# Performance work log

Measured on AMD Instinct MI355X. Metric: run time of the kernel, lower is better.

## Reference

```python
import jax, jax.numpy as jnp
import numpy as np

H = 1024
NH = 16
HD = H // NH

def setup_inputs() -> dict:
    key = jax.random.key(0)
    ks = jax.random.split(key, 8)
    s = 1.0 / np.sqrt(H)
    hidden_states = jax.random.normal(ks[0], (2, 2048, H), dtype=jnp.float32)
    attention_mask = jnp.zeros((2, 1, 1, 2048), dtype=jnp.float32)
    Wq = jax.random.uniform(ks[1], (H, H), jnp.float32, -s, s)
    bq = jax.random.uniform(ks[2], (H,), jnp.float32, -s, s)
    Wk = jax.random.uniform(ks[3], (H, H), jnp.float32, -s, s)
    bk = jax.random.uniform(ks[4], (H,), jnp.float32, -s, s)
    Wv = jax.random.uniform(ks[5], (H, H), jnp.float32, -s, s)
    bv = jax.random.uniform(ks[6], (H,), jnp.float32, -s, s)
    return {"hidden_states": hidden_states, "attention_mask": attention_mask,
            "Wq": Wq, "bq": bq, "Wk": Wk, "bk": bk, "Wv": Wv, "bv": bv}

def _split_heads(x):
    B, L, _ = x.shape
    return x.reshape(B, L, NH, HD).transpose(0, 2, 1, 3)  # [B, nh, L, hd]

def reference(hidden_states, attention_mask, Wq, bq, Wk, bk, Wv, bv):
    # QKV projections (nn.Linear: x @ W.T + b)
    Q = _split_heads(hidden_states @ Wq.T + bq)
    K = _split_heads(hidden_states @ Wk.T + bk)
    V = _split_heads(hidden_states @ Wv.T + bv)
    scale = 1.0 / np.sqrt(HD)
    scores = jnp.einsum('bhqd,bhkd->bhqk', Q, K) * scale  # [B, nh, L, L]
    scores = scores + attention_mask
    probs = jax.nn.softmax(scores, axis=-1)  # dropout in eval mode = identity
    context = jnp.einsum('bhqk,bhkd->bhqd', probs, V)
    B, _, L, _ = context.shape
    return context.transpose(0, 2, 1, 3).reshape(B, L, H)
```

## Files before the change

kernel.cpp:

```cpp
#include <hip/hip_runtime.h>
#include <math.h>
#include <stdint.h>

#define H_DIM 1024
#define NH 16
#define HD 64
#define B_DIM 2
#define L_DIM 2048
#define M_TOT (B_DIM * L_DIM)

typedef __bf16 bf16_t;
typedef __bf16 bf16x8 __attribute__((ext_vector_type(8)));
typedef __bf16 bf16x4 __attribute__((ext_vector_type(4)));
typedef float  f32x4  __attribute__((ext_vector_type(4)));

#define AS1 const __attribute__((address_space(1))) void*
#define AS3 __attribute__((address_space(3))) void*

__global__ __launch_bounds__(256)
void cast_all(const float* __restrict__ x,
              const float* __restrict__ Wq, const float* __restrict__ Wk,
              const float* __restrict__ Wv, bf16_t* __restrict__ dst)
{
    const size_t idx = ((size_t)blockIdx.x * 256 + threadIdx.x) * 4;
    const float* src;
    size_t off;
    if (idx < (size_t)M_TOT * H_DIM) { src = x; off = idx; }
    else {
        size_t j = idx - (size_t)M_TOT * H_DIM;
        int z = (int)(j >> 20);
        off = j & ((1u << 20) - 1);
        src = (z == 0) ? Wq : (z == 1) ? Wk : Wv;
    }
    const float4 v = *(const float4*)(src + off);
    bf16x4 o;
    o[0] = (bf16_t)v.x; o[1] = (bf16_t)v.y;
    o[2] = (bf16_t)v.z; o[3] = (bf16_t)v.w;
    *(bf16x4*)(dst + idx) = o;
}

__global__ __launch_bounds__(256, 1)
void qkv_mfma(const bf16_t* __restrict__ xb, const bf16_t* __restrict__ wb,
              const float* __restrict__ bq, const float* __restrict__ bk,
              const float* __restrict__ bv,
              bf16_t* __restrict__ qb, bf16_t* __restrict__ kb,
              bf16_t* __restrict__ vt)
{
    __shared__ bf16_t As0[128 * 32];
    __shared__ bf16_t As1[128 * 32];
    __shared__ bf16_t As2[128 * 32];
    __shared__ bf16_t Bs0[3][128 * 32];
    __shared__ bf16_t Bs1[3][128 * 32];
    __shared__ bf16_t Bs2[3][128 * 32];

    const int tid = threadIdx.x;
    const int n   = blockIdx.x;
    const int bn  = (n & 7) * 128;
    const int bm  = (n >> 3) * 128;

    const int wave = tid >> 6;
    const int lane = tid & 63;
    const int lc   = lane & 15;
    const int quad = lane >> 4;
    const int wm   = wave >> 1;
    const int wn   = wave & 1;

    f32x4 acc[3][4][4];
    #pragma unroll
    for (int z = 0; z < 3; ++z)
        #pragma unroll
        for (int i = 0; i < 4; ++i)
            #pragma unroll
            for (int j = 0; j < 4; ++j)
                acc[z][i][j] = (f32x4){0.f, 0.f, 0.f, 0.f};

    const int srow = tid >> 2;
    const int sseg = tid & 3;
    const bf16_t* gA = xb + (size_t)(bm + srow) * H_DIM + (sseg ^ (srow & 3)) * 8;
    const bf16_t* gB = wb + (size_t)(bn + srow) * H_DIM + (sseg ^ (srow & 3)) * 8;
    const int woff = wave * 1024;

    auto stage = [&](int k0, bf16_t* A_, bf16_t (*B_)[128 * 32]) {
        __builtin_amdgcn_global_load_lds((AS1)(gA + k0),
            (AS3)((char*)A_ + woff), 16, 0, 0);
        __builtin_amdgcn_global_load_lds((AS1)(gA + k0 + (size_t)64 * H_DIM),
            (AS3)((char*)A_ + woff + 4096), 16, 0, 0);
        #pragma unroll
        for (int z = 0; z < 3; ++z) {
            const bf16_t* g = gB + (size_t)z * H_DIM * H_DIM + k0;
            __builtin_amdgcn_global_load_lds((AS1)(g),
                (AS3)((char*)B_[z] + woff), 16, 0, 0);
            __builtin_amdgcn_global_load_lds((AS1)(g + (size_t)64 * H_DIM),
                (AS3)((char*)B_[z] + woff + 4096), 16, 0, 0);
        }
    };

    const int slot = (quad ^ (lc & 3)) * 8;
    auto compute = [&](const bf16_t* A_, const bf16_t (*B_)[128 * 32]) {
        bf16x8 a[4];
        #pragma unroll
        for (int mi = 0; mi < 4; ++mi)
            a[mi] = *(const bf16x8*)(A_ + (wm * 64 + mi * 16 + lc) * 32 + slot);
        #pragma unroll
        for (int z = 0; z < 3; ++z) {
            bf16x8 b[4];
            #pragma unroll
            for (int ni = 0; ni < 4; ++ni)
                b[ni] = *(const bf16x8*)(B_[z] + (wn * 64 + ni * 16 + lc) * 32 + slot);
            #pragma unroll
            for (int mi = 0; mi < 4; ++mi)
                #pragma unroll
                for (int ni = 0; ni < 4; ++ni)
                    acc[z][mi][ni] = __builtin_amdgcn_mfma_f32_16x16x32_bf16(
                        a[mi], b[ni], acc[z][mi][ni], 0, 0, 0);
        }
    };

    auto step = [&](int kk, bf16_t* cA, bf16_t (*cB)[128 * 32],
                    bf16_t* nA, bf16_t (*nB)[128 * 32], bool doStage) {
        __builtin_amdgcn_s_waitcnt(0x0F78);
        __builtin_amdgcn_s_barrier();
        if (doStage) stage((kk + 2) * 32, nA, nB);
        compute(cA, cB);
    };

    stage(0,  As0, Bs0);
    stage(32, As1, Bs1);
    #pragma unroll 1
    for (int t = 0; t < 10; ++t) {
        const int kk = t * 3;
        step(kk,     As0, Bs0, As2, Bs2, true);
        step(kk + 1, As1, Bs1, As0, Bs0, true);
        step(kk + 2, As2, Bs2, As1, Bs1, true);
    }
    step(30, As0, Bs0, As2, Bs2, false);
    __builtin_amdgcn_s_waitcnt(0x0F70);
    __builtin_amdgcn_s_barrier();
    compute(As1, Bs1);

    const int nb = bn + wn * 64;
    #pragma unroll
    for (int z = 0; z < 3; ++z) {
        const float* bias = (z == 0) ? bq : (z == 1) ? bk : bv;
        float biasv[4];
        #pragma unroll
        for (int ni = 0; ni < 4; ++ni) biasv[ni] = bias[nb + ni * 16 + lc];

        #pragma unroll
        for (int mi = 0; mi < 4; ++mi) {
            const int m0 = bm + wm * 64 + mi * 16 + quad * 4;
            if (z == 2) {
                const int b_ = m0 >> 11;
                const int l0 = m0 & 2047;
                #pragma unroll
                for (int ni = 0; ni < 4; ++ni) {
                    const int nn = nb + ni * 16 + lc;
                    const int h = nn >> 6, d = nn & 63;
                    bf16x4 pk;
                    #pragma unroll
                    for (int r = 0; r < 4; ++r)
                        pk[r] = (bf16_t)(acc[z][mi][ni][r] + biasv[ni]);
                    *(bf16x4*)(vt + (((size_t)(b_ * NH + h)) * HD + d) * L_DIM + l0) = pk;
                }
            } else {
                bf16_t* dst = (z == 0) ? qb : kb;
                #pragma unroll
                for (int r = 0; r < 4; ++r) {
                    const int m  = m0 + r;
                    const int b_ = m >> 11;
                    const int l  = m & 2047;
                    #pragma unroll
                    for (int ni = 0; ni < 4; ++ni) {
                        const int nn = nb + ni * 16 + lc;
                        const int h = nn >> 6, d = nn & 63;
                        dst[(((size_t)(b_ * NH + h)) * L_DIM + l) * HD + d] =
                            (bf16_t)(acc[z][mi][ni][r] + biasv[ni]);
                    }
                }
            }
        }
    }
}

#define EXP_C   0.180336879f
#define LOG2E   1.442695041f
#define EXP_SH  11.541560327f

__device__ __forceinline__ void attn_tile32(
    int kbase, bool pre,
    const bf16_t* curK, const bf16_t* curV,
    bf16_t* nxtK, bf16_t* nxtV,
    const bf16_t* gK, const bf16_t* gV,
    bf16_t* Ps, const float* mrow, int lc, int quad,
    const bf16x8 (&bQ)[2][2], f32x4 (&o)[2][4], float (&rs)[2])
{
    __builtin_amdgcn_s_waitcnt(0x0F70);

    const int e = lc & 7;

    bf16x8 kf[2][2];
    #pragma unroll
    for (int ni = 0; ni < 2; ++ni) {
        const bf16_t* p = curK + (ni * 16 + lc) * 64;
        kf[ni][0] = *(const bf16x8*)(p + ((quad ^ e) << 3));
        kf[ni][1] = *(const bf16x8*)(p + (((quad ^ e) ^ 4) << 3));
    }

    if (pre) {
        const int nk = kbase + 32;
        #pragma unroll
        for (int i = 0; i < 4; ++i) {
            __builtin_amdgcn_global_load_lds(
                (AS1)(gK + (size_t)nk * 64 + i * 512),
                (AS3)(nxtK + i * 512), 16, 0, 0);
            __builtin_amdgcn_global_load_lds(
                (AS1)(gV + nk + i * 32768),
                (AS3)(nxtV + i * 512), 16, 0, 0);
        }
    }

    float mvs[2][4];
    #pragma unroll
    for (int ni = 0; ni < 2; ++ni) {
        const float4 mv = *(const float4*)(mrow + kbase + ni * 16 + quad * 4);
        mvs[ni][0] = mv.x * LOG2E - EXP_SH;
        mvs[ni][1] = mv.y * LOG2E - EXP_SH;
        mvs[ni][2] = mv.z * LOG2E - EXP_SH;
        mvs[ni][3] = mv.w * LOG2E - EXP_SH;
    }

    #pragma unroll
    for (int f = 0; f < 2; ++f) {
        f32x4 s[2];
        #pragma unroll
        for (int ni = 0; ni < 2; ++ni) {
            f32x4 t = (f32x4){0.f, 0.f, 0.f, 0.f};
            t = __builtin_amdgcn_mfma_f32_16x16x32_bf16(kf[ni][0], bQ[f][0], t, 0, 0, 0);
            t = __builtin_amdgcn_mfma_f32_16x16x32_bf16(kf[ni][1], bQ[f][1], t, 0, 0, 0);
            s[ni] = t;
        }
        float acc = 0.f;
        #pragma unroll
        for (int ni = 0; ni < 2; ++ni) {
            bf16x4 pk;
            #pragma unroll
            for (int r = 0; r < 4; ++r) {
                const float p = __builtin_amdgcn_exp2f(s[ni][r] * EXP_C + mvs[ni][r]);
                acc += p;
                pk[r] = (bf16_t)p;
            }
            const int c = f * 4 + ni * 2 + (quad >> 1);
            *(bf16x4*)(Ps + lc * 64 + ((c ^ e) << 3) + ((quad & 1) << 2)) = pk;
        }
        rs[f] += acc;
    }

    bf16x8 vf[4];
    const int e2 = lc >> 1;
    #pragma unroll
    for (int dg = 0; dg < 4; ++dg) {
        const int p  = dg * 8 + (lc >> 1);
        const int ch = (((lc & 1) << 2) + quad) ^ e2;
        vf[dg] = *(const bf16x8*)(curV + p * 64 + (ch << 3));
    }

    #pragma unroll
    for (int f = 0; f < 2; ++f) {
        const int c = f * 4 + quad;
        const bf16x8 bP = *(const bf16x8*)(Ps + lc * 64 + ((c ^ e) << 3));
        #pragma unroll
        for (int dg = 0; dg < 4; ++dg)
            o[f][dg] = __builtin_amdgcn_mfma_f32_16x16x32_bf16(vf[dg], bP, o[f][dg], 0, 0, 0);
    }
}

__global__ __launch_bounds__(64, 2)
void attn_mfma(const bf16_t* __restrict__ qb, const bf16_t* __restrict__ kb,
               const bf16_t* __restrict__ vt, const float* __restrict__ mask,
               float* __restrict__ out)
{
    __shared__ bf16_t Ks0[32 * 64];
    __shared__ bf16_t Ks1[32 * 64];
    __shared__ bf16_t Vs0[32 * 64];
    __shared__ bf16_t Vs1[32 * 64];
    __shared__ bf16_t Ps[16 * 64];

    const int lane = threadIdx.x & 63;
    const int lc   = lane & 15;
    const int quad = lane >> 4;
    const int rl   = lane >> 3;
    const int sg   = lane & 7;

    const int n    = blockIdx.x;
    const int bh   = (n & 7) * 4 + ((n >> 3) & 3);
    const int q0   = (n >> 5) * 32;
    const int b_   = bh >> 4;
    const int h    = bh & 15;

    bf16x8 bQ[2][2];
    #pragma unroll
    for (int f = 0; f < 2; ++f) {
        const bf16_t* Qp = qb + ((size_t)bh * L_DIM + q0 + f * 16 + lc) * HD + quad * 8;
        bQ[f][0] = *(const bf16x8*)(Qp);
        bQ[f][1] = *(const bf16x8*)(Qp + 32);
    }

    const bf16_t* Kbase = kb + (size_t)bh * L_DIM * HD;
    const bf16_t* Vbase = vt + (size_t)bh * HD * L_DIM;
    const float*  mrow  = mask + (size_t)b_ * L_DIM;

    const bf16_t* gK = Kbase + rl * 64 + (sg ^ rl) * 8;
    const int cV = sg ^ rl;
    const bf16_t* gV = Vbase + (size_t)(rl * 2 + (cV >> 2)) * L_DIM + (cV & 3) * 8;

    f32x4 o[2][4];
    #pragma unroll
    for (int f = 0; f < 2; ++f)
        #pragma unroll
        for (int dg = 0; dg < 4; ++dg) o[f][dg] = (f32x4){0.f, 0.f, 0.f, 0.f};
    float rs[2] = {0.f, 0.f};

    #pragma unroll
    for (int i = 0; i < 4; ++i) {
        __builtin_amdgcn_global_load_lds(
            (AS1)(gK + i * 512),
            (AS3)(Ks0 + i * 512), 16, 0, 0);
        __builtin_amdgcn_global_load_lds(
            (AS1)(gV + i * 32768),
            (AS3)(Vs0 + i * 512), 16, 0, 0);
    }

    #pragma unroll 1
    for (int t2 = 0; t2 < 32; ++t2) {
        const int kb0 = t2 * 64;
        attn_tile32(kb0,      true,     Ks0, Vs0, Ks1, Vs1, gK, gV, Ps,
                    mrow, lc, quad, bQ, o, rs);
        attn_tile32(kb0 + 32, t2 < 31,  Ks1, Vs1, Ks0, Vs0, gK, gV, Ps,
                    mrow, lc, quad, bQ, o, rs);
    }

    #pragma unroll
    for (int f = 0; f < 2; ++f) {
        float l = rs[f];
        l += __shfl_xor(l, 16);
        l += __shfl_xor(l, 32);
        const float inv = 1.0f / l;
        float* orow = out + ((size_t)(b_ * L_DIM + q0 + f * 16 + lc)) * H_DIM
                    + h * HD + quad * 4;
        #pragma unroll
        for (int dg = 0; dg < 4; ++dg) {
            f32x4 w = o[f][dg];
            w[0] *= inv; w[1] *= inv; w[2] *= inv; w[3] *= inv;
            *(f32x4*)(orow + dg * 16) = w;
        }
    }
}

extern "C" void kernel_launch(void* const* d_in, const int* in_sizes, int n_in,
                              void* d_out, int out_size, void* d_ws, size_t ws_size,
                              hipStream_t stream) {
    const float* hidden = (const float*)d_in[0];
    const float* mask   = (const float*)d_in[1];
    const float* Wq     = (const float*)d_in[2];
    const float* bq     = (const float*)d_in[3];
    const float* Wk     = (const float*)d_in[4];
    const float* bk     = (const float*)d_in[5];
    const float* Wv     = (const float*)d_in[6];
    const float* bv     = (const float*)d_in[7];
    float* out = (float*)d_out;

    const size_t XN = (size_t)M_TOT * H_DIM;
    const size_t WN = (size_t)3 * H_DIM * H_DIM;
    bf16_t* xwb = (bf16_t*)d_ws;
    bf16_t* qb  = xwb + XN + WN;
    bf16_t* kb  = qb + XN;
    bf16_t* vt  = kb + XN;

    cast_all<<<(int)((XN + WN) / 1024), 256, 0, stream>>>(hidden, Wq, Wk, Wv, xwb);

    qkv_mfma<<<256, 256, 0, stream>>>(xwb, xwb + XN, bq, bk, bv, qb, kb, vt);

    attn_mfma<<<2048, 64, 0, stream>>>(qb, kb, vt, mask, out);
}
```

Before: 181.9 us.

## Split attention keys across two halves and share K/V tiles between two waves

The attention kernel becomes 128-thread blocks. Each block has two waves covering 64 queries, and the two waves cooperatively load shared K/V tiles into LDS, synchronised with a barrier. Each block now handles only half of the key range (split-K), writing unnormalised partial outputs and row sums to workspace. A new combine kernel adds the two halves and normalises. This halves per-wave K/V loading and keeps the grid size, at the cost of an extra kernel launch, extra global traffic for the partials, and per-tile barriers. The softmax uses a fixed exponent shift with no running max, so the split is exact.

```diff
diff --git a/kernel.cpp b/kernel.cpp
--- a/kernel.cpp
+++ b/kernel.cpp
@@ -190,11 +190,12 @@
     int kbase, bool pre,
     const bf16_t* curK, const bf16_t* curV,
     bf16_t* nxtK, bf16_t* nxtV,
-    const bf16_t* gK, const bf16_t* gV,
+    const bf16_t* gKw, const bf16_t* gVw, int wo,
     bf16_t* Ps, const float* mrow, int lc, int quad,
     const bf16x8 (&bQ)[2][2], f32x4 (&o)[2][4], float (&rs)[2])
 {
     __builtin_amdgcn_s_waitcnt(0x0F70);
+    __builtin_amdgcn_s_barrier();
 
     const int e = lc & 7;
 
@@ -209,13 +210,13 @@
     if (pre) {
         const int nk = kbase + 32;
         #pragma unroll
-        for (int i = 0; i < 4; ++i) {
+        for (int i = 0; i < 2; ++i) {
             __builtin_amdgcn_global_load_lds(
-                (AS1)(gK + (size_t)nk * 64 + i * 512),
-                (AS3)(nxtK + i * 512), 16, 0, 0);
+                (AS1)(gKw + (size_t)nk * 64 + i * 512),
+                (AS3)(nxtK + wo + i * 512), 16, 0, 0);
             __builtin_amdgcn_global_load_lds(
-                (AS1)(gV + nk + i * 32768),
-                (AS3)(nxtV + i * 512), 16, 0, 0);
+                (AS1)(gVw + nk + (size_t)i * 32768),
+                (AS3)(nxtV + wo + i * 512), 16, 0, 0);
         }
     }
 
@@ -274,18 +275,21 @@
     }
 }
 
-__global__ __launch_bounds__(64, 2)
+__global__ __launch_bounds__(128, 4)
 void attn_mfma(const bf16_t* __restrict__ qb, const bf16_t* __restrict__ kb,
                const bf16_t* __restrict__ vt, const float* __restrict__ mask,
-               float* __restrict__ out)
+               float* __restrict__ out, float* __restrict__ o1,
+               float* __restrict__ l0, float* __restrict__ l1)
 {
     __shared__ bf16_t Ks0[32 * 64];
     __shared__ bf16_t Ks1[32 * 64];
     __shared__ bf16_t Vs0[32 * 64];
     __shared__ bf16_t Vs1[32 * 64];
-    __shared__ bf16_t Ps[16 * 64];
-
-    const int lane = threadIdx.x & 63;
+    __shared__ bf16_t Ps[2][16 * 64];
+
+    const int tid  = threadIdx.x;
+    const int wave = tid >> 6;
+    const int lane = tid & 63;
     const int lc   = lane & 15;
     const int quad = lane >> 4;
     const int rl   = lane >> 3;
@@ -293,9 +297,13 @@
 
     const int n    = blockIdx.x;
     const int bh   = (n & 7) * 4 + ((n >> 3) & 3);
-    const int q0   = (n >> 5) * 32;
+    const int q0   = ((n >> 5) & 31) * 64 + wave * 32;
+    const int kh   = (n >> 10) & 1;
+    const int k0   = kh << 10;
     const int b_   = bh >> 4;
     const int h    = bh & 15;
+
+    bf16_t* Psw = Ps[wave];
 
     bf16x8 bQ[2][2];
     #pragma unroll
@@ -307,11 +315,14 @@
 
     const bf16_t* Kbase = kb + (size_t)bh * L_DIM * HD;
     const bf16_t* Vbase = vt + (size_t)bh * HD * L_DIM;
-    const float*  mrow  = mask + (size_t)b_ * L_DIM;
-
-    const bf16_t* gK = Kbase + rl * 64 + (sg ^ rl) * 8;
+    const float*  mrow  = mask + (size_t)b_ * L_DIM + k0;
+
     const int cV = sg ^ rl;
-    const bf16_t* gV = Vbase + (size_t)(rl * 2 + (cV >> 2)) * L_DIM + (cV & 3) * 8;
+    const bf16_t* gKw = Kbase + (size_t)(k0 + rl) * 64 + (sg ^ rl) * 8
+                      + (size_t)wave * 1024;
+    const bf16_t* gVw = Vbase + k0 + (size_t)(rl * 2 + (cV >> 2)) * L_DIM
+                      + (cV & 3) * 8 + (size_t)wave * 65536;
+    const int wo = wave * 1024;
 
     f32x4 o[2][4];
     #pragma unroll
@@ -321,39 +332,58 @@
     float rs[2] = {0.f, 0.f};
 
     #pragma unroll
-    for (int i = 0; i < 4; ++i) {
+    for (int i = 0; i < 2; ++i) {
         __builtin_amdgcn_global_load_lds(
-            (AS1)(gK + i * 512),
-            (AS3)(Ks0 + i * 512), 16, 0, 0);
+            (AS1)(gKw + i * 512),
+            (AS3)(Ks0 + wo + i * 512), 16, 0, 0);
         __builtin_amdgcn_global_load_lds(
-            (AS1)(gV + i * 32768),
-            (AS3)(Vs0 + i * 512), 16, 0, 0);
+            (AS1)(gVw + (size_t)i * 32768),
+            (AS3)(Vs0 + wo + i * 512), 16, 0, 0);
     }
 
     #pragma unroll 1
-    for (int t2 = 0; t2 < 32; ++t2) {
+    for (int t2 = 0; t2 < 16; ++t2) {
         const int kb0 = t2 * 64;
-        attn_tile32(kb0,      true,     Ks0, Vs0, Ks1, Vs1, gK, gV, Ps,
+        attn_tile32(kb0,      true,     Ks0, Vs0, Ks1, Vs1, gKw, gVw, wo, Psw,
                     mrow, lc, quad, bQ, o, rs);
-        attn_tile32(kb0 + 32, t2 < 31,  Ks1, Vs1, Ks0, Vs0, gK, gV, Ps,
+        attn_tile32(kb0 + 32, t2 < 15,  Ks1, Vs1, Ks0, Vs0, gKw, gVw, wo, Psw,
                     mrow, lc, quad, bQ, o, rs);
     }
 
+    float* obase = (kh == 0) ? out : o1;
+    float* lbase = (kh == 0) ? l0  : l1;
     #pragma unroll
     for (int f = 0; f < 2; ++f) {
         float l = rs[f];
         l += __shfl_xor(l, 16);
         l += __shfl_xor(l, 32);
-        const float inv = 1.0f / l;
-        float* orow = out + ((size_t)(b_ * L_DIM + q0 + f * 16 + lc)) * H_DIM
+        if (quad == 0)
+            lbase[(size_t)bh * L_DIM + q0 + f * 16 + lc] = l;
+        float* orow = obase + ((size_t)(b_ * L_DIM + q0 + f * 16 + lc)) * H_DIM
                     + h * HD + quad * 4;
         #pragma unroll
-        for (int dg = 0; dg < 4; ++dg) {
-            f32x4 w = o[f][dg];
-            w[0] *= inv; w[1] *= inv; w[2] *= inv; w[3] *= inv;
-            *(f32x4*)(orow + dg * 16) = w;
-        }
-    }
+        for (int dg = 0; dg < 4; ++dg)
+            *(f32x4*)(orow + dg * 16) = o[f][dg];
+    }
+}
+
+__global__ __launch_bounds__(256)
+void attn_combine(const float* __restrict__ o1,
+                  const float* __restrict__ l0, const float* __restrict__ l1,
+                  float* __restrict__ out)
+{
+    const size_t idx = ((size_t)blockIdx.x * 256 + threadIdx.x) * 4;
+    const int m   = (int)(idx >> 10);
+    const int col = (int)(idx & 1023);
+    const int b_  = m >> 11;
+    const int q   = m & 2047;
+    const int h   = col >> 6;
+    const size_t lidx = ((size_t)(b_ * NH + h)) * L_DIM + q;
+    const float inv = 1.0f / (l0[lidx] + l1[lidx]);
+    f32x4 a = *(const f32x4*)(out + idx);
+    const f32x4 b = *(const f32x4*)(o1 + idx);
+    a = (a + b) * inv;
+    *(f32x4*)(out + idx) = a;
 }
 
 extern "C" void kernel_launch(void* const* d_in, const int* in_sizes, int n_in,
@@ -375,10 +405,15 @@
     bf16_t* qb  = xwb + XN + WN;
     bf16_t* kb  = qb + XN;
     bf16_t* vt  = kb + XN;
+    float*  o1  = (float*)(vt + XN);
+    float*  l0  = o1 + XN;
+    float*  l1  = l0 + (size_t)B_DIM * NH * L_DIM;
 
     cast_all<<<(int)((XN + WN) / 1024), 256, 0, stream>>>(hidden, Wq, Wk, Wv, xwb);
 
     qkv_mfma<<<256, 256, 0, stream>>>(xwb, xwb + XN, bq, bk, bv, qb, kb, vt);
 
-    attn_mfma<<<2048, 64, 0, stream>>>(qb, kb, vt, mask, out);
-}
+    attn_mfma<<<2048, 128, 0, stream>>>(qb, kb, vt, mask, out, o1, l0, l1);
+
+    attn_combine<<<4096, 256, 0, stream>>>(o1, l0, l1, out);
+}
```

After: 177.5 us. -2.4%, faster.
